# Optimization experiments

Hardware: AMD Instinct MI355X
Metric: run time of the kernel (lower is better)

## Reference

```python
import jax, jax.numpy as jnp
import numpy as np

N_NODES = 50000
N_EDGES = 600000
C_IN = 128
C_HID = 256
EPS = 1e-5  # InstanceNorm1d default eps


def setup_inputs() -> dict:
    key = jax.random.key(0)
    ks = jax.random.split(key, 12)
    node_features = jax.random.normal(ks[0], (N_NODES, C_IN), dtype=jnp.float32)
    edge_features = jax.random.normal(ks[1], (N_EDGES, C_IN), dtype=jnp.float32)
    edge_index = jax.random.randint(ks[2], (2, N_EDGES), 0, N_NODES, dtype=jnp.int64)
    s1 = 1.0 / np.sqrt(C_IN)
    s2 = 1.0 / np.sqrt(C_HID)
    # FCNN_one params (acts on summed node features)
    W1a = jax.random.uniform(ks[3], (C_IN, C_HID), jnp.float32, -s1, s1)
    b1a = jax.random.uniform(ks[4], (C_HID,), jnp.float32, -s1, s1)
    W2a = jax.random.uniform(ks[5], (C_HID, C_IN), jnp.float32, -s2, s2)
    b2a = jax.random.uniform(ks[6], (C_IN,), jnp.float32, -s2, s2)
    # FCNN_two params (acts on edge features)
    W1b = jax.random.uniform(ks[7], (C_IN, C_HID), jnp.float32, -s1, s1)
    b1b = jax.random.uniform(ks[8], (C_HID,), jnp.float32, -s1, s1)
    W2b = jax.random.uniform(ks[9], (C_HID, C_IN), jnp.float32, -s2, s2)
    b2b = jax.random.uniform(ks[10], (C_IN,), jnp.float32, -s2, s2)
    return {
        "node_features": node_features,
        "edge_features": edge_features,
        "edge_index": edge_index,
        "W1a": W1a, "b1a": b1a, "W2a": W2a, "b2a": b2a,
        "W1b": W1b, "b1b": b1b, "W2b": W2b, "b2b": b2b,
    }


def reference(node_features, edge_features, edge_index,
              W1a, b1a, W2a, b2a, W1b, b1b, W2b, b2b):
    src, dst = edge_index[0], edge_index[1]
    # gather node pairs and sum: [E, C_IN]
    s = node_features[src] + node_features[dst]
    # FCNN_one on node sums
    hn = jnp.maximum(s @ W1a + b1a, 0.0) @ W2a + b2a
    # FCNN_two on edge features
    he = jnp.maximum(edge_features @ W1b + b1b, 0.0) @ W2b + b2b
    h = hn + he  # [E, C_IN]
    # InstanceNorm1d on a (1, C) reshape == normalize each edge's feature vector
    mu = jnp.mean(h, axis=-1, keepdims=True)
    var = jnp.mean(jnp.square(h - mu), axis=-1, keepdims=True)  # biased variance
    h = (h - mu) * jax.lax.rsqrt(var + EPS)
    # dropout in eval mode = identity; relu; residual with original edge features
    return edge_features + jnp.maximum(h, 0.0)
```

## Files before the change

kernel.cpp:

```cpp
#include <hip/hip_runtime.h>
#include <stdint.h>
#include <stddef.h>

#define NE 600000
#define NN 50000
#define CI 128
#define CH 256
#define EPSI 1e-5f

typedef __attribute__((ext_vector_type(8))) short bf8;
typedef __attribute__((ext_vector_type(4))) float f4;
typedef __attribute__((ext_vector_type(4))) unsigned int u4;

union FragU { bf8 h; uint32_t w[4]; };

__device__ __forceinline__ unsigned short f2bf(float f) {
  union { float f; uint32_t u; } v; v.f = f;
  uint32_t u = v.u;
  u += 0x7FFFu + ((u >> 16) & 1u);
  return (unsigned short)(u >> 16);
}

__device__ __forceinline__ uint32_t cvtpk(float lo, float hi) {
  uint32_t r;
  asm("v_cvt_pk_bf16_f32 %0, %1, %2" : "=v"(r) : "v"(lo), "v"(hi));
  return r;
}

__device__ __forceinline__ float asf(uint32_t x) {
  union { uint32_t u; float f; } v; v.u = x; return v.f;
}

__global__ void pack_weights(const float* __restrict__ W1a, const float* __restrict__ W1b,
                             const float* __restrict__ W2a, const float* __restrict__ W2b,
                             unsigned short* __restrict__ ws) {
  int i = blockIdx.x * 256 + threadIdx.x;
  if (i >= 4 * 32768) return;
  int m = i >> 15;
  int r = i & 32767;
  int j = r & 7;
  int l = (r >> 3) & 63;
  int kg = l >> 4, q = l & 15;
  float val;
  if (m < 2) {
    int t = (r >> 9) & 3;
    int tau = (r >> 11) & 1;
    int c = (r >> 12) & 7;
    int cin = 32 * t + kg * 8 + j;
    int hid = 32 * c + 8 * (q >> 2) + 4 * tau + (q & 3);
    const float* W1 = (m == 0) ? W1a : W1b;
    val = W1[cin * CH + hid];
  } else {
    int c = (r >> 9) & 7;
    int mt = (r >> 12) & 7;
    int hid = 32 * c + kg * 8 + j;
    int cout = 16 * mt + q;
    const float* W2 = (m == 2) ? W2a : W2b;
    val = W2[hid * CI + cout];
  }
  ws[(size_t)m * 32768 + r] = f2bf(val);
}

__global__ __launch_bounds__(256)
void node_pre(const float* __restrict__ node, const float* __restrict__ b1a,
              const unsigned short* __restrict__ wp, unsigned short* __restrict__ Ua) {
  const int tid = threadIdx.x;
  const int lane = tid & 63;
  const int wv = tid >> 6;
  const int kg = lane >> 4, ar = lane & 15;
  const int n0 = blockIdx.x * 64 + wv * 16 + ar;
  const bool okn = (n0 < NN);
  const int n = okn ? n0 : (NN - 1);
  const float* pn = node + (size_t)n * CI;

  FragU xn[4];
#pragma unroll
  for (int t = 0; t < 4; ++t) {
    const int c0 = t * 32 + kg * 8;
    f4 v0 = *(const f4*)(pn + c0);
    f4 v1 = *(const f4*)(pn + c0 + 4);
    xn[t].w[0] = cvtpk(v0[0], v0[1]); xn[t].w[1] = cvtpk(v0[2], v0[3]);
    xn[t].w[2] = cvtpk(v1[0], v1[1]); xn[t].w[3] = cvtpk(v1[2], v1[3]);
  }
  const int lofs = lane * 8;
#pragma unroll 1
  for (int c = 0; c < 8; ++c) {
    f4 t0 = *(const f4*)(b1a + c * 32 + kg * 8) * 0.5f;
    f4 t1 = *(const f4*)(b1a + c * 32 + kg * 8 + 4) * 0.5f;
    const unsigned short* p1 = wp + c * 4096;
#pragma unroll
    for (int t = 0; t < 4; ++t) {
      bf8 a0 = *(const bf8*)(p1 + t * 512 + lofs);
      bf8 a1 = *(const bf8*)(p1 + 2048 + t * 512 + lofs);
      t0 = __builtin_amdgcn_mfma_f32_16x16x32_bf16(a0, xn[t].h, t0, 0, 0, 0);
      t1 = __builtin_amdgcn_mfma_f32_16x16x32_bf16(a1, xn[t].h, t1, 0, 0, 0);
    }
    u4 q;
    q[0] = cvtpk(t0[0], t0[1]); q[1] = cvtpk(t0[2], t0[3]);
    q[2] = cvtpk(t1[0], t1[1]); q[3] = cvtpk(t1[2], t1[3]);
    if (okn) *(u4*)(Ua + (size_t)n * CH + c * 32 + kg * 8) = q;
  }
}

__global__ __launch_bounds__(1024, 4)
void edge_fused(const unsigned short* __restrict__ Ua,
                const float* __restrict__ ef,
                const int* __restrict__ eidx,
                const float* __restrict__ b1b,
                const float* __restrict__ b2a, const float* __restrict__ b2b,
                const unsigned short* __restrict__ wp,
                float* __restrict__ out) {
  __shared__ __align__(16) unsigned short lw[65536];
  const int tid = threadIdx.x;
  const int lane = tid & 63;
  const int wv = tid >> 6;
  const int kg = lane >> 4, ar = lane & 15;
  const int lofs = lane * 8;

  {
    const u4* s1 = (const u4*)(wp + 32768);
    const u4* s2 = (const u4*)(wp + 98304);
    u4* l = (u4*)lw;
#pragma unroll
    for (int i = 0; i < 4; ++i) {
      int o = i * 1024 + tid;
      l[o] = s1[o];
      l[4096 + o] = s2[o];
    }
  }

  const int be = blockIdx.x * 512 + wv * 32;
  const int e0 = be + ar, e1 = be + 16 + ar;
  const int ec0 = (e0 < NE) ? e0 : (NE - 1);
  const int ec1 = (e1 < NE) ? e1 : (NE - 1);

  f4 hacc[2][8];
#pragma unroll
  for (int mt = 0; mt < 8; ++mt) {
    f4 u = *(const f4*)(b2a + mt * 16 + kg * 4);
    f4 v = *(const f4*)(b2b + mt * 16 + kg * 4);
    hacc[0][mt] = u + v;
    hacc[1][mt] = u + v;
  }

  {
    const unsigned short* pUs0 = Ua + (size_t)eidx[ec0] * CH;
    const unsigned short* pUd0 = Ua + (size_t)eidx[NE + ec0] * CH;
    const unsigned short* pUs1 = Ua + (size_t)eidx[ec1] * CH;
    const unsigned short* pUd1 = Ua + (size_t)eidx[NE + ec1] * CH;
    const unsigned short* P2a = wp + 65536;
#pragma unroll 1
    for (int u = 0; u < 8; ++u) {
      const int ko = u * 32 + kg * 8;
      u4 a0 = *(const u4*)(pUs0 + ko), d0 = *(const u4*)(pUd0 + ko);
      u4 a1 = *(const u4*)(pUs1 + ko), d1 = *(const u4*)(pUd1 + ko);
      FragU tb0, tb1;
#pragma unroll
      for (int i = 0; i < 4; ++i) {
        float lo0 = asf(a0[i] << 16) + asf(d0[i] << 16);
        float hi0 = asf(a0[i] & 0xFFFF0000u) + asf(d0[i] & 0xFFFF0000u);
        tb0.w[i] = cvtpk(fmaxf(lo0, 0.f), fmaxf(hi0, 0.f));
        float lo1 = asf(a1[i] << 16) + asf(d1[i] << 16);
        float hi1 = asf(a1[i] & 0xFFFF0000u) + asf(d1[i] & 0xFFFF0000u);
        tb1.w[i] = cvtpk(fmaxf(lo1, 0.f), fmaxf(hi1, 0.f));
      }
#pragma unroll
      for (int mt = 0; mt < 8; ++mt) {
        bf8 a = *(const bf8*)(P2a + (mt * 8 + u) * 512 + lofs);
        hacc[0][mt] = __builtin_amdgcn_mfma_f32_16x16x32_bf16(a, tb0.h, hacc[0][mt], 0, 0, 0);
        hacc[1][mt] = __builtin_amdgcn_mfma_f32_16x16x32_bf16(a, tb1.h, hacc[1][mt], 0, 0, 0);
      }
    }
  }

  __syncthreads();

#pragma unroll
  for (int g = 0; g < 2; ++g) {
    const int ecg = g ? ec1 : ec0;
    const float* pe = ef + (size_t)ecg * CI;
    FragU xe[4];
#pragma unroll
    for (int t = 0; t < 4; ++t) {
      const int c0 = t * 32 + kg * 8;
      f4 v0 = *(const f4*)(pe + c0);
      f4 v1 = *(const f4*)(pe + c0 + 4);
      xe[t].w[0] = cvtpk(v0[0], v0[1]); xe[t].w[1] = cvtpk(v0[2], v0[3]);
      xe[t].w[2] = cvtpk(v1[0], v1[1]); xe[t].w[3] = cvtpk(v1[2], v1[3]);
    }
#pragma unroll 1
    for (int c = 0; c < 8; ++c) {
      f4 t0 = *(const f4*)(b1b + c * 32 + kg * 8);
      f4 t1 = *(const f4*)(b1b + c * 32 + kg * 8 + 4);
#pragma unroll
      for (int t = 0; t < 4; ++t) {
        bf8 a0 = *(const bf8*)(lw + c * 4096 + t * 512 + lofs);
        bf8 a1 = *(const bf8*)(lw + c * 4096 + 2048 + t * 512 + lofs);
        t0 = __builtin_amdgcn_mfma_f32_16x16x32_bf16(a0, xe[t].h, t0, 0, 0, 0);
        t1 = __builtin_amdgcn_mfma_f32_16x16x32_bf16(a1, xe[t].h, t1, 0, 0, 0);
      }
      FragU bf_;
      bf_.w[0] = cvtpk(fmaxf(t0[0], 0.f), fmaxf(t0[1], 0.f));
      bf_.w[1] = cvtpk(fmaxf(t0[2], 0.f), fmaxf(t0[3], 0.f));
      bf_.w[2] = cvtpk(fmaxf(t1[0], 0.f), fmaxf(t1[1], 0.f));
      bf_.w[3] = cvtpk(fmaxf(t1[2], 0.f), fmaxf(t1[3], 0.f));
#pragma unroll
      for (int mt = 0; mt < 8; ++mt) {
        bf8 a2 = *(const bf8*)(lw + 32768 + (mt * 8 + c) * 512 + lofs);
        hacc[g][mt] = __builtin_amdgcn_mfma_f32_16x16x32_bf16(a2, bf_.h, hacc[g][mt], 0, 0, 0);
      }
    }
  }

#pragma unroll
  for (int g = 0; g < 2; ++g) {
    float sum = 0.f, sq = 0.f;
#pragma unroll
    for (int mt = 0; mt < 8; ++mt)
#pragma unroll
      for (int i = 0; i < 4; ++i) { float v = hacc[g][mt][i]; sum += v; sq += v * v; }
    sum += __shfl_xor(sum, 16); sum += __shfl_xor(sum, 32);
    sq  += __shfl_xor(sq, 16);  sq  += __shfl_xor(sq, 32);
    const float mu = sum * (1.0f / 128.0f);
    const float var = sq * (1.0f / 128.0f) - mu * mu;
    const float rs = rsqrtf(var + EPSI);
    const int e = g ? e1 : e0;
    if (e < NE) {
      float* po = out + (size_t)e * CI;
      const float* pr = ef + (size_t)e * CI;
#pragma unroll
      for (int mt = 0; mt < 8; ++mt) {
        f4 r = *(const f4*)(pr + mt * 16 + kg * 4);
        f4 o;
#pragma unroll
        for (int i = 0; i < 4; ++i) {
          float n = (hacc[g][mt][i] - mu) * rs;
          o[i] = r[i] + fmaxf(n, 0.f);
        }
        *(f4*)(po + mt * 16 + kg * 4) = o;
      }
    }
  }
}

extern "C" void kernel_launch(void* const* d_in, const int* in_sizes, int n_in,
                              void* d_out, int out_size, void* d_ws, size_t ws_size,
                              hipStream_t stream) {
  const float* node = (const float*)d_in[0];
  const float* ef   = (const float*)d_in[1];
  const int* eidx   = (const int*)d_in[2];
  const float* W1a = (const float*)d_in[3];
  const float* b1a = (const float*)d_in[4];
  const float* W2a = (const float*)d_in[5];
  const float* b2a = (const float*)d_in[6];
  const float* W1b = (const float*)d_in[7];
  const float* b1b = (const float*)d_in[8];
  const float* W2b = (const float*)d_in[9];
  const float* b2b = (const float*)d_in[10];
  unsigned short* wp = (unsigned short*)d_ws;
  unsigned short* Ua = wp + 131072;
  float* outp = (float*)d_out;

  pack_weights<<<512, 256, 0, stream>>>(W1a, W1b, W2a, W2b, wp);
  node_pre<<<(NN + 63) / 64, 256, 0, stream>>>(node, b1a, wp, Ua);
  edge_fused<<<(NE + 511) / 512, 1024, 0, stream>>>(
      Ua, ef, eidx, b1b, b2a, b2b, wp, outp);
}
```

Measured before the change: 361.7 us.

## Stage only W2a in LDS, halve block size, read edge MLP weights from global

The edge kernel now stages only the W2a fragment (64 KB) in LDS instead of W1b and W2b (128 KB). W1b and W2b are read straight from global memory, and the W2a node-sum GEMM that used to read global now reads LDS. Blocks drop from 1024 to 512 threads covering 256 edges, and the node-gather loop is fully unrolled over both edge groups. The aim is to cut LDS use per block so more blocks fit per CU and the staging load per block shrinks. The cost is that the 16 edge-MLP weight MFMAs per step now fetch from L2/global, and the full unroll raises register pressure.

```diff
diff --git a/kernel.cpp b/kernel.cpp
--- a/kernel.cpp
+++ b/kernel.cpp
@@ -102,7 +102,7 @@
   }
 }
 
-__global__ __launch_bounds__(1024, 4)
+__global__ __launch_bounds__(512, 4)
 void edge_fused(const unsigned short* __restrict__ Ua,
                 const float* __restrict__ ef,
                 const int* __restrict__ eidx,
@@ -110,7 +110,7 @@
                 const float* __restrict__ b2a, const float* __restrict__ b2b,
                 const unsigned short* __restrict__ wp,
                 float* __restrict__ out) {
-  __shared__ __align__(16) unsigned short lw[65536];
+  __shared__ __align__(16) unsigned short lw[32768];
   const int tid = threadIdx.x;
   const int lane = tid & 63;
   const int wv = tid >> 6;
@@ -118,21 +118,24 @@
   const int lofs = lane * 8;
 
   {
-    const u4* s1 = (const u4*)(wp + 32768);
-    const u4* s2 = (const u4*)(wp + 98304);
+    const u4* s2 = (const u4*)(wp + 65536);
     u4* l = (u4*)lw;
 #pragma unroll
-    for (int i = 0; i < 4; ++i) {
-      int o = i * 1024 + tid;
-      l[o] = s1[o];
-      l[4096 + o] = s2[o];
-    }
-  }
-
-  const int be = blockIdx.x * 512 + wv * 32;
+    for (int i = 0; i < 8; ++i) {
+      int o = i * 512 + tid;
+      l[o] = s2[o];
+    }
+  }
+
+  const int be = blockIdx.x * 256 + wv * 32;
   const int e0 = be + ar, e1 = be + 16 + ar;
   const int ec0 = (e0 < NE) ? e0 : (NE - 1);
   const int ec1 = (e1 < NE) ? e1 : (NE - 1);
+
+  const unsigned short* pUs0 = Ua + (size_t)eidx[ec0] * CH;
+  const unsigned short* pUd0 = Ua + (size_t)eidx[NE + ec0] * CH;
+  const unsigned short* pUs1 = Ua + (size_t)eidx[ec1] * CH;
+  const unsigned short* pUd1 = Ua + (size_t)eidx[NE + ec1] * CH;
 
   f4 hacc[2][8];
 #pragma unroll
@@ -143,37 +146,29 @@
     hacc[1][mt] = u + v;
   }
 
-  {
-    const unsigned short* pUs0 = Ua + (size_t)eidx[ec0] * CH;
-    const unsigned short* pUd0 = Ua + (size_t)eidx[NE + ec0] * CH;
-    const unsigned short* pUs1 = Ua + (size_t)eidx[ec1] * CH;
-    const unsigned short* pUd1 = Ua + (size_t)eidx[NE + ec1] * CH;
-    const unsigned short* P2a = wp + 65536;
-#pragma unroll 1
-    for (int u = 0; u < 8; ++u) {
-      const int ko = u * 32 + kg * 8;
-      u4 a0 = *(const u4*)(pUs0 + ko), d0 = *(const u4*)(pUd0 + ko);
-      u4 a1 = *(const u4*)(pUs1 + ko), d1 = *(const u4*)(pUd1 + ko);
-      FragU tb0, tb1;
-#pragma unroll
-      for (int i = 0; i < 4; ++i) {
-        float lo0 = asf(a0[i] << 16) + asf(d0[i] << 16);
-        float hi0 = asf(a0[i] & 0xFFFF0000u) + asf(d0[i] & 0xFFFF0000u);
-        tb0.w[i] = cvtpk(fmaxf(lo0, 0.f), fmaxf(hi0, 0.f));
-        float lo1 = asf(a1[i] << 16) + asf(d1[i] << 16);
-        float hi1 = asf(a1[i] & 0xFFFF0000u) + asf(d1[i] & 0xFFFF0000u);
-        tb1.w[i] = cvtpk(fmaxf(lo1, 0.f), fmaxf(hi1, 0.f));
-      }
-#pragma unroll
-      for (int mt = 0; mt < 8; ++mt) {
-        bf8 a = *(const bf8*)(P2a + (mt * 8 + u) * 512 + lofs);
-        hacc[0][mt] = __builtin_amdgcn_mfma_f32_16x16x32_bf16(a, tb0.h, hacc[0][mt], 0, 0, 0);
-        hacc[1][mt] = __builtin_amdgcn_mfma_f32_16x16x32_bf16(a, tb1.h, hacc[1][mt], 0, 0, 0);
-      }
-    }
-  }
-
   __syncthreads();
+
+#pragma unroll
+  for (int s = 0; s < 16; ++s) {
+    const int u = s >> 1, g = s & 1;
+    const unsigned short* ps = g ? pUs1 : pUs0;
+    const unsigned short* pd = g ? pUd1 : pUd0;
+    const int ko = u * 32 + kg * 8;
+    u4 av = *(const u4*)(ps + ko);
+    u4 dv = *(const u4*)(pd + ko);
+    FragU tb;
+#pragma unroll
+    for (int i = 0; i < 4; ++i) {
+      float lo = asf(av[i] << 16) + asf(dv[i] << 16);
+      float hi = asf(av[i] & 0xFFFF0000u) + asf(dv[i] & 0xFFFF0000u);
+      tb.w[i] = cvtpk(fmaxf(lo, 0.f), fmaxf(hi, 0.f));
+    }
+#pragma unroll
+    for (int mt = 0; mt < 8; ++mt) {
+      bf8 a2 = *(const bf8*)(lw + (mt * 8 + u) * 512 + lofs);
+      hacc[g][mt] = __builtin_amdgcn_mfma_f32_16x16x32_bf16(a2, tb.h, hacc[g][mt], 0, 0, 0);
+    }
+  }
 
 #pragma unroll
   for (int g = 0; g < 2; ++g) {
@@ -188,14 +183,16 @@
       xe[t].w[0] = cvtpk(v0[0], v0[1]); xe[t].w[1] = cvtpk(v0[2], v0[3]);
       xe[t].w[2] = cvtpk(v1[0], v1[1]); xe[t].w[3] = cvtpk(v1[2], v1[3]);
     }
+    const unsigned short* P1b = wp + 32768;
+    const unsigned short* P2b = wp + 98304;
 #pragma unroll 1
     for (int c = 0; c < 8; ++c) {
       f4 t0 = *(const f4*)(b1b + c * 32 + kg * 8);
       f4 t1 = *(const f4*)(b1b + c * 32 + kg * 8 + 4);
 #pragma unroll
       for (int t = 0; t < 4; ++t) {
-        bf8 a0 = *(const bf8*)(lw + c * 4096 + t * 512 + lofs);
-        bf8 a1 = *(const bf8*)(lw + c * 4096 + 2048 + t * 512 + lofs);
+        bf8 a0 = *(const bf8*)(P1b + c * 4096 + t * 512 + lofs);
+        bf8 a1 = *(const bf8*)(P1b + c * 4096 + 2048 + t * 512 + lofs);
         t0 = __builtin_amdgcn_mfma_f32_16x16x32_bf16(a0, xe[t].h, t0, 0, 0, 0);
         t1 = __builtin_amdgcn_mfma_f32_16x16x32_bf16(a1, xe[t].h, t1, 0, 0, 0);
       }
@@ -206,7 +203,7 @@
       bf_.w[3] = cvtpk(fmaxf(t1[2], 0.f), fmaxf(t1[3], 0.f));
 #pragma unroll
       for (int mt = 0; mt < 8; ++mt) {
-        bf8 a2 = *(const bf8*)(lw + 32768 + (mt * 8 + c) * 512 + lofs);
+        bf8 a2 = *(const bf8*)(P2b + (mt * 8 + c) * 512 + lofs);
         hacc[g][mt] = __builtin_amdgcn_mfma_f32_16x16x32_bf16(a2, bf_.h, hacc[g][mt], 0, 0, 0);
       }
     }
@@ -263,6 +260,6 @@
 
   pack_weights<<<512, 256, 0, stream>>>(W1a, W1b, W2a, W2b, wp);
   node_pre<<<(NN + 63) / 64, 256, 0, stream>>>(node, b1a, wp, Ua);
-  edge_fused<<<(NE + 511) / 512, 1024, 0, stream>>>(
+  edge_fused<<<(NE + 255) / 256, 512, 0, stream>>>(
       Ua, ef, eidx, b1b, b2a, b2b, wp, outp);
 }
```

After: 484.8 us. 1.34x slower.

## Interleave gathered node-sum MFMAs with edge MLP and prefetch gathers two steps ahead

Applied to the files above, without the earlier changes.

Restructures the per-wave work so each 16-edge group runs the edge-feature MLP chunk and the gathered node-hidden GEMM chunk inside the same loop iteration. The gathered Ua rows are software-prefetched two K-steps ahead, continuing into the next group's rows, so random-gather latency hides behind MFMA work. Accumulators drop from two groups to one, which cuts register pressure and may raise occupancy. Groups are processed one after another, so the earlier two-group MFMA parallelism is lost.

```diff
diff --git a/kernel.cpp b/kernel.cpp
--- a/kernel.cpp
+++ b/kernel.cpp
@@ -133,53 +133,16 @@
   const int e0 = be + ar, e1 = be + 16 + ar;
   const int ec0 = (e0 < NE) ? e0 : (NE - 1);
   const int ec1 = (e1 < NE) ? e1 : (NE - 1);
-
-  f4 hacc[2][8];
-#pragma unroll
-  for (int mt = 0; mt < 8; ++mt) {
-    f4 u = *(const f4*)(b2a + mt * 16 + kg * 4);
-    f4 v = *(const f4*)(b2b + mt * 16 + kg * 4);
-    hacc[0][mt] = u + v;
-    hacc[1][mt] = u + v;
-  }
-
-  {
-    const unsigned short* pUs0 = Ua + (size_t)eidx[ec0] * CH;
-    const unsigned short* pUd0 = Ua + (size_t)eidx[NE + ec0] * CH;
-    const unsigned short* pUs1 = Ua + (size_t)eidx[ec1] * CH;
-    const unsigned short* pUd1 = Ua + (size_t)eidx[NE + ec1] * CH;
-    const unsigned short* P2a = wp + 65536;
-#pragma unroll 1
-    for (int u = 0; u < 8; ++u) {
-      const int ko = u * 32 + kg * 8;
-      u4 a0 = *(const u4*)(pUs0 + ko), d0 = *(const u4*)(pUd0 + ko);
-      u4 a1 = *(const u4*)(pUs1 + ko), d1 = *(const u4*)(pUd1 + ko);
-      FragU tb0, tb1;
-#pragma unroll
-      for (int i = 0; i < 4; ++i) {
-        float lo0 = asf(a0[i] << 16) + asf(d0[i] << 16);
-        float hi0 = asf(a0[i] & 0xFFFF0000u) + asf(d0[i] & 0xFFFF0000u);
-        tb0.w[i] = cvtpk(fmaxf(lo0, 0.f), fmaxf(hi0, 0.f));
-        float lo1 = asf(a1[i] << 16) + asf(d1[i] << 16);
-        float hi1 = asf(a1[i] & 0xFFFF0000u) + asf(d1[i] & 0xFFFF0000u);
-        tb1.w[i] = cvtpk(fmaxf(lo1, 0.f), fmaxf(hi1, 0.f));
-      }
-#pragma unroll
-      for (int mt = 0; mt < 8; ++mt) {
-        bf8 a = *(const bf8*)(P2a + (mt * 8 + u) * 512 + lofs);
-        hacc[0][mt] = __builtin_amdgcn_mfma_f32_16x16x32_bf16(a, tb0.h, hacc[0][mt], 0, 0, 0);
-        hacc[1][mt] = __builtin_amdgcn_mfma_f32_16x16x32_bf16(a, tb1.h, hacc[1][mt], 0, 0, 0);
-      }
-    }
-  }
-
-  __syncthreads();
-
-#pragma unroll
-  for (int g = 0; g < 2; ++g) {
-    const int ecg = g ? ec1 : ec0;
-    const float* pe = ef + (size_t)ecg * CI;
-    FragU xe[4];
+  const unsigned short* pUs0 = Ua + (size_t)eidx[ec0] * CH;
+  const unsigned short* pUd0 = Ua + (size_t)eidx[NE + ec0] * CH;
+  const unsigned short* pUs1 = Ua + (size_t)eidx[ec1] * CH;
+  const unsigned short* pUd1 = Ua + (size_t)eidx[NE + ec1] * CH;
+
+  FragU xe[4];
+  f4 hacc[8];
+  u4 avb[2], dvb[2];
+
+  auto ldxe = [&](const float* pe) {
 #pragma unroll
     for (int t = 0; t < 4; ++t) {
       const int c0 = t * 32 + kg * 8;
@@ -188,8 +151,30 @@
       xe[t].w[0] = cvtpk(v0[0], v0[1]); xe[t].w[1] = cvtpk(v0[2], v0[3]);
       xe[t].w[2] = cvtpk(v1[0], v1[1]); xe[t].w[3] = cvtpk(v1[2], v1[3]);
     }
-#pragma unroll 1
+  };
+
+  auto hinit = [&]() {
+#pragma unroll
+    for (int mt = 0; mt < 8; ++mt) {
+      f4 u = *(const f4*)(b2a + mt * 16 + kg * 4);
+      f4 v = *(const f4*)(b2b + mt * 16 + kg * 4);
+      hacc[mt] = u + v;
+    }
+  };
+
+  auto rungrp = [&](const unsigned short* pUs, const unsigned short* pUd,
+                    const unsigned short* pUsN, const unsigned short* pUdN) {
+    const unsigned short* P2a = wp + 65536;
+#pragma unroll
     for (int c = 0; c < 8; ++c) {
+      u4 avN = {}, dvN = {};
+      if (c < 6) {
+        avN = *(const u4*)(pUs + (c + 2) * 32 + kg * 8);
+        dvN = *(const u4*)(pUd + (c + 2) * 32 + kg * 8);
+      } else if (pUsN) {
+        avN = *(const u4*)(pUsN + (c - 6) * 32 + kg * 8);
+        dvN = *(const u4*)(pUdN + (c - 6) * 32 + kg * 8);
+      }
       f4 t0 = *(const f4*)(b1b + c * 32 + kg * 8);
       f4 t1 = *(const f4*)(b1b + c * 32 + kg * 8 + 4);
 #pragma unroll
@@ -207,24 +192,38 @@
 #pragma unroll
       for (int mt = 0; mt < 8; ++mt) {
         bf8 a2 = *(const bf8*)(lw + 32768 + (mt * 8 + c) * 512 + lofs);
-        hacc[g][mt] = __builtin_amdgcn_mfma_f32_16x16x32_bf16(a2, bf_.h, hacc[g][mt], 0, 0, 0);
-      }
-    }
-  }
-
-#pragma unroll
-  for (int g = 0; g < 2; ++g) {
+        hacc[mt] = __builtin_amdgcn_mfma_f32_16x16x32_bf16(a2, bf_.h, hacc[mt], 0, 0, 0);
+      }
+      {
+        u4 av = avb[c & 1], dv = dvb[c & 1];
+        FragU tb;
+#pragma unroll
+        for (int i = 0; i < 4; ++i) {
+          float lo = asf(av[i] << 16) + asf(dv[i] << 16);
+          float hi = asf(av[i] & 0xFFFF0000u) + asf(dv[i] & 0xFFFF0000u);
+          tb.w[i] = cvtpk(fmaxf(lo, 0.f), fmaxf(hi, 0.f));
+        }
+#pragma unroll
+        for (int mt = 0; mt < 8; ++mt) {
+          bf8 aW = *(const bf8*)(P2a + (mt * 8 + c) * 512 + lofs);
+          hacc[mt] = __builtin_amdgcn_mfma_f32_16x16x32_bf16(aW, tb.h, hacc[mt], 0, 0, 0);
+        }
+      }
+      avb[c & 1] = avN; dvb[c & 1] = dvN;
+    }
+  };
+
+  auto phaseC = [&](int e) {
     float sum = 0.f, sq = 0.f;
 #pragma unroll
     for (int mt = 0; mt < 8; ++mt)
 #pragma unroll
-      for (int i = 0; i < 4; ++i) { float v = hacc[g][mt][i]; sum += v; sq += v * v; }
+      for (int i = 0; i < 4; ++i) { float v = hacc[mt][i]; sum += v; sq += v * v; }
     sum += __shfl_xor(sum, 16); sum += __shfl_xor(sum, 32);
     sq  += __shfl_xor(sq, 16);  sq  += __shfl_xor(sq, 32);
     const float mu = sum * (1.0f / 128.0f);
     const float var = sq * (1.0f / 128.0f) - mu * mu;
     const float rs = rsqrtf(var + EPSI);
-    const int e = g ? e1 : e0;
     if (e < NE) {
       float* po = out + (size_t)e * CI;
       const float* pr = ef + (size_t)e * CI;
@@ -234,13 +233,28 @@
         f4 o;
 #pragma unroll
         for (int i = 0; i < 4; ++i) {
-          float n = (hacc[g][mt][i] - mu) * rs;
+          float n = (hacc[mt][i] - mu) * rs;
           o[i] = r[i] + fmaxf(n, 0.f);
         }
         *(f4*)(po + mt * 16 + kg * 4) = o;
       }
     }
-  }
+  };
+
+  ldxe(ef + (size_t)ec0 * CI);
+  hinit();
+  avb[0] = *(const u4*)(pUs0 + kg * 8);
+  dvb[0] = *(const u4*)(pUd0 + kg * 8);
+  avb[1] = *(const u4*)(pUs0 + 32 + kg * 8);
+  dvb[1] = *(const u4*)(pUd0 + 32 + kg * 8);
+  __syncthreads();
+
+  rungrp(pUs0, pUd0, pUs1, pUd1);
+  ldxe(ef + (size_t)ec1 * CI);
+  phaseC(e0);
+  hinit();
+  rungrp(pUs1, pUd1, nullptr, nullptr);
+  phaseC(e1);
 }
 
 extern "C" void kernel_launch(void* const* d_in, const int* in_sizes, int n_in,
```

New measurement: 684.7 us. +89.3%, slower.

## Interleave edge MLP with software-pipelined node gathers, one edge group per wave

Applied to the files above, without the earlier changes.

Each wave now handles 16 edges instead of 32, and the grid doubles to match. The gathers of the precomputed node hidden rows are issued two steps ahead and interleaved with the edge-feature dense MLP chunks. The aim is to hide gather latency behind MFMA work rather than waiting on it in a separate loop. The trade-off is that every block reloads the 128KB of LDS weights, so with twice as many blocks that staging traffic doubles, and register pressure changes.

```diff
diff --git a/kernel.cpp b/kernel.cpp
--- a/kernel.cpp
+++ b/kernel.cpp
@@ -102,6 +102,45 @@
   }
 }
 
+#define ISSUE(Sv, Dv, u) \
+  Sv = *(const u4*)(pUs + (u) * 32 + kg * 8); \
+  Dv = *(const u4*)(pUd + (u) * 32 + kg * 8);
+
+#define DENSE(c) { \
+  f4 t0 = *(const f4*)(b1b + (c) * 32 + kg * 8); \
+  f4 t1 = *(const f4*)(b1b + (c) * 32 + kg * 8 + 4); \
+  _Pragma("unroll") \
+  for (int t = 0; t < 4; ++t) { \
+    bf8 a0 = *(const bf8*)(lw + (c) * 4096 + t * 512 + lofs); \
+    bf8 a1 = *(const bf8*)(lw + (c) * 4096 + 2048 + t * 512 + lofs); \
+    t0 = __builtin_amdgcn_mfma_f32_16x16x32_bf16(a0, xe[t].h, t0, 0, 0, 0); \
+    t1 = __builtin_amdgcn_mfma_f32_16x16x32_bf16(a1, xe[t].h, t1, 0, 0, 0); \
+  } \
+  FragU bf_; \
+  bf_.w[0] = cvtpk(fmaxf(t0[0], 0.f), fmaxf(t0[1], 0.f)); \
+  bf_.w[1] = cvtpk(fmaxf(t0[2], 0.f), fmaxf(t0[3], 0.f)); \
+  bf_.w[2] = cvtpk(fmaxf(t1[0], 0.f), fmaxf(t1[1], 0.f)); \
+  bf_.w[3] = cvtpk(fmaxf(t1[2], 0.f), fmaxf(t1[3], 0.f)); \
+  _Pragma("unroll") \
+  for (int mt = 0; mt < 8; ++mt) { \
+    bf8 a2 = *(const bf8*)(lw + 32768 + (mt * 8 + (c)) * 512 + lofs); \
+    hacc[mt] = __builtin_amdgcn_mfma_f32_16x16x32_bf16(a2, bf_.h, hacc[mt], 0, 0, 0); \
+  } }
+
+#define CONS(Sv, Dv, u) { \
+  FragU tb; \
+  _Pragma("unroll") \
+  for (int i = 0; i < 4; ++i) { \
+    float lo = asf(Sv[i] << 16) + asf(Dv[i] << 16); \
+    float hi = asf(Sv[i] & 0xFFFF0000u) + asf(Dv[i] & 0xFFFF0000u); \
+    tb.w[i] = cvtpk(fmaxf(lo, 0.f), fmaxf(hi, 0.f)); \
+  } \
+  _Pragma("unroll") \
+  for (int mt = 0; mt < 8; ++mt) { \
+    bf8 aW = *(const bf8*)(P2a + (mt * 8 + (u)) * 512 + lofs); \
+    hacc[mt] = __builtin_amdgcn_mfma_f32_16x16x32_bf16(aW, tb.h, hacc[mt], 0, 0, 0); \
+  } }
+
 __global__ __launch_bounds__(1024, 4)
 void edge_fused(const unsigned short* __restrict__ Ua,
                 const float* __restrict__ ef,
@@ -117,6 +156,13 @@
   const int kg = lane >> 4, ar = lane & 15;
   const int lofs = lane * 8;
 
+  const int e = blockIdx.x * 256 + wv * 16 + ar;
+  const int ec = (e < NE) ? e : (NE - 1);
+  const int is = eidx[ec], id = eidx[NE + ec];
+  const unsigned short* pUs = Ua + (size_t)is * CH;
+  const unsigned short* pUd = Ua + (size_t)id * CH;
+  const unsigned short* P2a = wp + 65536;
+
   {
     const u4* s1 = (const u4*)(wp + 32768);
     const u4* s2 = (const u4*)(wp + 98304);
@@ -129,102 +175,50 @@
     }
   }
 
-  const int be = blockIdx.x * 512 + wv * 32;
-  const int e0 = be + ar, e1 = be + 16 + ar;
-  const int ec0 = (e0 < NE) ? e0 : (NE - 1);
-  const int ec1 = (e1 < NE) ? e1 : (NE - 1);
-
-  f4 hacc[2][8];
+  const float* pe = ef + (size_t)ec * CI;
+  FragU xe[4];
+#pragma unroll
+  for (int t = 0; t < 4; ++t) {
+    const int c0 = t * 32 + kg * 8;
+    f4 v0 = *(const f4*)(pe + c0);
+    f4 v1 = *(const f4*)(pe + c0 + 4);
+    xe[t].w[0] = cvtpk(v0[0], v0[1]); xe[t].w[1] = cvtpk(v0[2], v0[3]);
+    xe[t].w[2] = cvtpk(v1[0], v1[1]); xe[t].w[3] = cvtpk(v1[2], v1[3]);
+  }
+
+  f4 hacc[8];
 #pragma unroll
   for (int mt = 0; mt < 8; ++mt) {
     f4 u = *(const f4*)(b2a + mt * 16 + kg * 4);
     f4 v = *(const f4*)(b2b + mt * 16 + kg * 4);
-    hacc[0][mt] = u + v;
-    hacc[1][mt] = u + v;
-  }
+    hacc[mt] = u + v;
+  }
+
+  __syncthreads();
+
+  u4 As, Ad, Bs, Bd;
+  ISSUE(As, Ad, 0)
+  ISSUE(Bs, Bd, 1)
+  DENSE(0) CONS(As, Ad, 0) ISSUE(As, Ad, 2)
+  DENSE(1) CONS(Bs, Bd, 1) ISSUE(Bs, Bd, 3)
+  DENSE(2) CONS(As, Ad, 2) ISSUE(As, Ad, 4)
+  DENSE(3) CONS(Bs, Bd, 3) ISSUE(Bs, Bd, 5)
+  DENSE(4) CONS(As, Ad, 4) ISSUE(As, Ad, 6)
+  DENSE(5) CONS(Bs, Bd, 5) ISSUE(Bs, Bd, 7)
+  DENSE(6) CONS(As, Ad, 6)
+  DENSE(7) CONS(Bs, Bd, 7)
 
   {
-    const unsigned short* pUs0 = Ua + (size_t)eidx[ec0] * CH;
-    const unsigned short* pUd0 = Ua + (size_t)eidx[NE + ec0] * CH;
-    const unsigned short* pUs1 = Ua + (size_t)eidx[ec1] * CH;
-    const unsigned short* pUd1 = Ua + (size_t)eidx[NE + ec1] * CH;
-    const unsigned short* P2a = wp + 65536;
-#pragma unroll 1
-    for (int u = 0; u < 8; ++u) {
-      const int ko = u * 32 + kg * 8;
-      u4 a0 = *(const u4*)(pUs0 + ko), d0 = *(const u4*)(pUd0 + ko);
-      u4 a1 = *(const u4*)(pUs1 + ko), d1 = *(const u4*)(pUd1 + ko);
-      FragU tb0, tb1;
-#pragma unroll
-      for (int i = 0; i < 4; ++i) {
-        float lo0 = asf(a0[i] << 16) + asf(d0[i] << 16);
-        float hi0 = asf(a0[i] & 0xFFFF0000u) + asf(d0[i] & 0xFFFF0000u);
-        tb0.w[i] = cvtpk(fmaxf(lo0, 0.f), fmaxf(hi0, 0.f));
-        float lo1 = asf(a1[i] << 16) + asf(d1[i] << 16);
-        float hi1 = asf(a1[i] & 0xFFFF0000u) + asf(d1[i] & 0xFFFF0000u);
-        tb1.w[i] = cvtpk(fmaxf(lo1, 0.f), fmaxf(hi1, 0.f));
-      }
-#pragma unroll
-      for (int mt = 0; mt < 8; ++mt) {
-        bf8 a = *(const bf8*)(P2a + (mt * 8 + u) * 512 + lofs);
-        hacc[0][mt] = __builtin_amdgcn_mfma_f32_16x16x32_bf16(a, tb0.h, hacc[0][mt], 0, 0, 0);
-        hacc[1][mt] = __builtin_amdgcn_mfma_f32_16x16x32_bf16(a, tb1.h, hacc[1][mt], 0, 0, 0);
-      }
-    }
-  }
-
-  __syncthreads();
-
-#pragma unroll
-  for (int g = 0; g < 2; ++g) {
-    const int ecg = g ? ec1 : ec0;
-    const float* pe = ef + (size_t)ecg * CI;
-    FragU xe[4];
-#pragma unroll
-    for (int t = 0; t < 4; ++t) {
-      const int c0 = t * 32 + kg * 8;
-      f4 v0 = *(const f4*)(pe + c0);
-      f4 v1 = *(const f4*)(pe + c0 + 4);
-      xe[t].w[0] = cvtpk(v0[0], v0[1]); xe[t].w[1] = cvtpk(v0[2], v0[3]);
-      xe[t].w[2] = cvtpk(v1[0], v1[1]); xe[t].w[3] = cvtpk(v1[2], v1[3]);
-    }
-#pragma unroll 1
-    for (int c = 0; c < 8; ++c) {
-      f4 t0 = *(const f4*)(b1b + c * 32 + kg * 8);
-      f4 t1 = *(const f4*)(b1b + c * 32 + kg * 8 + 4);
-#pragma unroll
-      for (int t = 0; t < 4; ++t) {
-        bf8 a0 = *(const bf8*)(lw + c * 4096 + t * 512 + lofs);
-        bf8 a1 = *(const bf8*)(lw + c * 4096 + 2048 + t * 512 + lofs);
-        t0 = __builtin_amdgcn_mfma_f32_16x16x32_bf16(a0, xe[t].h, t0, 0, 0, 0);
-        t1 = __builtin_amdgcn_mfma_f32_16x16x32_bf16(a1, xe[t].h, t1, 0, 0, 0);
-      }
-      FragU bf_;
-      bf_.w[0] = cvtpk(fmaxf(t0[0], 0.f), fmaxf(t0[1], 0.f));
-      bf_.w[1] = cvtpk(fmaxf(t0[2], 0.f), fmaxf(t0[3], 0.f));
-      bf_.w[2] = cvtpk(fmaxf(t1[0], 0.f), fmaxf(t1[1], 0.f));
-      bf_.w[3] = cvtpk(fmaxf(t1[2], 0.f), fmaxf(t1[3], 0.f));
-#pragma unroll
-      for (int mt = 0; mt < 8; ++mt) {
-        bf8 a2 = *(const bf8*)(lw + 32768 + (mt * 8 + c) * 512 + lofs);
-        hacc[g][mt] = __builtin_amdgcn_mfma_f32_16x16x32_bf16(a2, bf_.h, hacc[g][mt], 0, 0, 0);
-      }
-    }
-  }
-
-#pragma unroll
-  for (int g = 0; g < 2; ++g) {
     float sum = 0.f, sq = 0.f;
 #pragma unroll
     for (int mt = 0; mt < 8; ++mt)
 #pragma unroll
-      for (int i = 0; i < 4; ++i) { float v = hacc[g][mt][i]; sum += v; sq += v * v; }
+      for (int i = 0; i < 4; ++i) { float v = hacc[mt][i]; sum += v; sq += v * v; }
     sum += __shfl_xor(sum, 16); sum += __shfl_xor(sum, 32);
     sq  += __shfl_xor(sq, 16);  sq  += __shfl_xor(sq, 32);
     const float mu = sum * (1.0f / 128.0f);
     const float var = sq * (1.0f / 128.0f) - mu * mu;
     const float rs = rsqrtf(var + EPSI);
-    const int e = g ? e1 : e0;
     if (e < NE) {
       float* po = out + (size_t)e * CI;
       const float* pr = ef + (size_t)e * CI;
@@ -234,7 +228,7 @@
         f4 o;
 #pragma unroll
         for (int i = 0; i < 4; ++i) {
-          float n = (hacc[g][mt][i] - mu) * rs;
+          float n = (hacc[mt][i] - mu) * rs;
           o[i] = r[i] + fmaxf(n, 0.f);
         }
         *(f4*)(po + mt * 16 + kg * 4) = o;
@@ -263,6 +257,6 @@
 
   pack_weights<<<512, 256, 0, stream>>>(W1a, W1b, W2a, W2b, wp);
   node_pre<<<(NN + 63) / 64, 256, 0, stream>>>(node, b1a, wp, Ua);
-  edge_fused<<<(NE + 511) / 512, 1024, 0, stream>>>(
+  edge_fused<<<(NE + 255) / 256, 1024, 0, stream>>>(
       Ua, ef, eidx, b1b, b2a, b2b, wp, outp);
 }
```

Result: slower. 369.6 us (+2.2%).
